# Kernel optimization log

Measured on AMD Instinct MI355X. Metric: run time of the kernel, lower is better.

The kernel has to match this reference:

```python
import jax, jax.numpy as jnp
import numpy as np

LEVELS = [(128, 128), (64, 64), (32, 32), (16, 16)]  # (H_l, W_l) per feature level
N_TOTAL = sum(h * w for h, w in LEVELS)  # 21760
B, D, H, P, L = 2, 256, 8, 4, 4
HD = D // H
FFN_DIM = 1024


def setup_inputs() -> dict:
    key = jax.random.key(0)
    ks = jax.random.split(key, 12)
    s = 0.02  # weight init scale
    return {
        'embed': jax.random.normal(ks[0], (B, N_TOTAL, D), jnp.float32),
        'pos': jax.random.normal(ks[1], (B, N_TOTAL, D), jnp.float32),
        'ref_points': jax.random.uniform(ks[2], (B, N_TOTAL, L, 2), jnp.float32),
        'ln1_w': jnp.ones((D,), jnp.float32), 'ln1_b': jnp.zeros((D,), jnp.float32),
        'ln2_w': jnp.ones((D,), jnp.float32), 'ln2_b': jnp.zeros((D,), jnp.float32),
        'Wv': jax.random.normal(ks[3], (D, D), jnp.float32) * s, 'bv': jnp.zeros((D,), jnp.float32),
        'Woff': jax.random.normal(ks[4], (D, H * L * P * 2), jnp.float32) * s, 'boff': jnp.zeros((H * L * P * 2,), jnp.float32),
        'Wattn': jax.random.normal(ks[5], (D, H * L * P), jnp.float32) * s, 'battn': jnp.zeros((H * L * P,), jnp.float32),
        'Wo': jax.random.normal(ks[6], (D, D), jnp.float32) * s, 'bo': jnp.zeros((D,), jnp.float32),
        'W1': jax.random.normal(ks[7], (D, FFN_DIM), jnp.float32) * s, 'b1': jnp.zeros((FFN_DIM,), jnp.float32),
        'W2': jax.random.normal(ks[8], (FFN_DIM, D), jnp.float32) * s, 'b2': jnp.zeros((D,), jnp.float32),
        'dimensions': jnp.array(LEVELS, jnp.int32),
    }


def _layer_norm(x, w, b):
    m = jnp.mean(x, axis=-1, keepdims=True)
    v = jnp.mean(jnp.square(x - m), axis=-1, keepdims=True)
    return (x - m) * jax.lax.rsqrt(v + 1e-5) * w + b


def _msda(q, ref, v, dims, Wv, bv, Woff, boff, Wattn, battn, Wo, bo):
    # q, v: (B, N, D); ref: (B, N, L, 2) normalized (x, y)
    Bq, N, _ = q.shape
    value = (v @ Wv + bv).reshape(Bq, N, H, HD)
    off = (q @ Woff + boff).reshape(Bq, N, H, L, P, 2)
    aw = jax.nn.softmax((q @ Wattn + battn).reshape(Bq, N, H, L * P), axis=-1)
    aw = aw.reshape(Bq, N, H, L, P)
    # offset normalizer is [W_l, H_l]
    norm = jnp.stack([dims[:, 1], dims[:, 0]], axis=-1).astype(q.dtype)  # (L, 2)
    loc = ref[:, :, None, :, None, :] + off / norm[None, None, None, :, None, :]  # (B,N,H,L,P,2)

    out = jnp.zeros((Bq, N, H, HD), q.dtype)
    start = 0
    for l, (Hl, Wl) in enumerate(LEVELS):
        S = Hl * Wl
        vl = value[:, start:start + S].transpose(0, 2, 1, 3)  # (B, H, S, hd)
        start += S
        # grid_sample semantics: align_corners=False, zero padding
        x = loc[:, :, :, l, :, 0] * Wl - 0.5  # (B, N, H, P)
        y = loc[:, :, :, l, :, 1] * Hl - 0.5
        x0 = jnp.floor(x); y0 = jnp.floor(y)
        wx = x - x0; wy = y - y0
        x0i = x0.astype(jnp.int32); y0i = y0.astype(jnp.int32)
        samp = jnp.zeros(x.shape + (HD,), q.dtype)
        for dy, dx, w in ((0, 0, (1 - wx) * (1 - wy)), (0, 1, wx * (1 - wy)),
                          (1, 0, (1 - wx) * wy), (1, 1, wx * wy)):
            xi = x0i + dx; yi = y0i + dy
            valid = (xi >= 0) & (xi < Wl) & (yi >= 0) & (yi < Hl)
            idx = jnp.clip(yi, 0, Hl - 1) * Wl + jnp.clip(xi, 0, Wl - 1)  # (B, N, H, P)
            idx_t = idx.transpose(0, 2, 1, 3).reshape(Bq, H, N * P)
            g = jnp.take_along_axis(vl, idx_t[..., None], axis=2)  # (B, H, N*P, hd)
            g = g.reshape(Bq, H, N, P, HD).transpose(0, 2, 1, 3, 4)  # (B, N, H, P, hd)
            samp = samp + (w * valid)[..., None] * g
        out = out + jnp.sum(samp * aw[:, :, :, l, :, None], axis=3)
    return out.reshape(Bq, N, D) @ Wo + bo


def reference(embed, pos, ref_points, ln1_w, ln1_b, ln2_w, ln2_b, Wv, bv, Woff, boff,
              Wattn, battn, Wo, bo, W1, b1, W2, b2, dimensions):
    v = _layer_norm(embed, ln1_w, ln1_b)
    q = v + pos
    embed = embed + _msda(q, ref_points, v, dimensions, Wv, bv, Woff, boff, Wattn, battn, Wo, bo)
    f = _layer_norm(embed, ln2_w, ln2_b)
    embed = embed + jax.nn.relu(f @ W1 + b1) @ W2 + b2
    return embed
```

## Files before the change

### kernel.cpp

```cpp
#include <hip/hip_runtime.h>
#include <cstdint>
#include <cstddef>

#define N_TOTAL 21760
#define BATCH   2
#define M_TOT   (BATCH * N_TOTAL)
#define DMODEL  256
#define NHEAD   8
#define HDIM    32
#define FFN     1024

typedef __bf16 b16x8 __attribute__((ext_vector_type(8)));
typedef float  f32x4 __attribute__((ext_vector_type(4)));

typedef const __attribute__((address_space(1))) void g_void;
typedef __attribute__((address_space(3))) void lds_void;

__device__ __forceinline__ unsigned short f2b(float f) {
  union { float f; unsigned u; } v; v.f = f;
  unsigned r = v.u + 0x7FFF + ((v.u >> 16) & 1);
  return (unsigned short)(r >> 16);
}
__device__ __forceinline__ float b2f(unsigned short u) {
  union { unsigned u; float f; } v; v.u = (unsigned)u << 16;
  return v.f;
}

__device__ __forceinline__ int xcd_wgid(int bid, int nwg) {
  int q = nwg >> 3, r = nwg & 7;
  int xcd = bid & 7, k = bid >> 3;
  return (xcd < r ? xcd * (q + 1) : r * (q + 1) + (xcd - r) * q) + k;
}

__global__ void wconv_all(const float* __restrict__ Wv, const float* __restrict__ Woff,
                          const float* __restrict__ Wattn, const float* __restrict__ Wo,
                          const float* __restrict__ W1, const float* __restrict__ W2,
                          unsigned short* __restrict__ dstbase) {
  int idx = blockIdx.x * 256 + threadIdx.x;
  const float* src; int K, N, off;
  if (idx < 65536)       { src = Wv;    K = 256;  N = 256;  off = 0;      }
  else if (idx < 131072) { src = Woff;  K = 256;  N = 256;  off = 65536;  idx -= 65536; }
  else if (idx < 163840) { src = Wattn; K = 256;  N = 128;  off = 131072; idx -= 131072; }
  else if (idx < 229376) { src = Wo;    K = 256;  N = 256;  off = 163840; idx -= 163840; }
  else if (idx < 491520) { src = W1;    K = 256;  N = 1024; off = 229376; idx -= 229376; }
  else if (idx < 753664) { src = W2;    K = 1024; N = 256;  off = 491520; idx -= 491520; }
  else return;
  int k = idx / N, n = idx - k * N;
  dstbase[off + (size_t)n * K + k] = f2b(src[idx]);
}

__global__ void ln1_kernel(const float* __restrict__ x, const float* __restrict__ pos,
                           const float* __restrict__ w, const float* __restrict__ b,
                           unsigned short* __restrict__ vb, unsigned short* __restrict__ qb) {
  int t = threadIdx.x;
  int tkn = blockIdx.x * 4 + (t >> 6);
  int lane = t & 63;
  size_t base = (size_t)tkn * DMODEL + lane * 4;
  float4 xv = *(const float4*)&x[base];
  float s1 = xv.x + xv.y + xv.z + xv.w;
  float s2 = xv.x * xv.x + xv.y * xv.y + xv.z * xv.z + xv.w * xv.w;
  #pragma unroll
  for (int off = 32; off; off >>= 1) {
    s1 += __shfl_down(s1, off);
    s2 += __shfl_down(s2, off);
  }
  s1 = __shfl(s1, 0); s2 = __shfl(s2, 0);
  float m   = s1 * (1.0f / DMODEL);
  float var = s2 * (1.0f / DMODEL) - m * m;
  float rs  = rsqrtf(var + 1e-5f);
  float4 wv = *(const float4*)&w[lane * 4];
  float4 bv = *(const float4*)&b[lane * 4];
  float4 pv = *(const float4*)&pos[base];
  float o0 = (xv.x - m) * rs * wv.x + bv.x;
  float o1 = (xv.y - m) * rs * wv.y + bv.y;
  float o2 = (xv.z - m) * rs * wv.z + bv.z;
  float o3 = (xv.w - m) * rs * wv.w + bv.w;
  ushort4 vo = {f2b(o0), f2b(o1), f2b(o2), f2b(o3)};
  ushort4 qo = {f2b(o0 + pv.x), f2b(o1 + pv.y), f2b(o2 + pv.z), f2b(o3 + pv.w)};
  *(ushort4*)&vb[base] = vo;
  *(ushort4*)&qb[base] = qo;
}

__device__ __forceinline__ void gemm_core(
    const unsigned short* __restrict__ A, const unsigned short* __restrict__ Bt,
    const float* __restrict__ bias,
    const float* __restrict__ addf, const unsigned short* __restrict__ addb,
    float* __restrict__ Cf, unsigned short* __restrict__ Cb,
    int K, int N, int relu, int row0, int col0,
    unsigned short* As, unsigned short* Bs) {
  int t  = threadIdx.x;
  int w  = t >> 6;
  int l  = t & 63;
  int wm = w >> 1, wn = w & 1;
  int lr = l & 15;
  int kq = l >> 4;

  f32x4 acc[4][4];
  #pragma unroll
  for (int i = 0; i < 4; ++i)
    #pragma unroll
    for (int j = 0; j < 4; ++j) acc[i][j] = (f32x4){0.f, 0.f, 0.f, 0.f};

  int srow = (l >> 3);
  int sseg = (l & 7) * 8;

  for (int k0 = 0; k0 < K; k0 += 64) {
    #pragma unroll
    for (int i = 0; i < 4; ++i) {
      int c = w * 4 + i;
      const unsigned short* ga = A  + (size_t)(row0 + c * 8 + srow) * K + k0 + sseg;
      const unsigned short* gb = Bt + (size_t)(col0 + c * 8 + srow) * K + k0 + sseg;
      __builtin_amdgcn_global_load_lds((g_void*)ga, (lds_void*)(As + c * 512), 16, 0, 0);
      __builtin_amdgcn_global_load_lds((g_void*)gb, (lds_void*)(Bs + c * 512), 16, 0, 0);
    }
    __syncthreads();
    #pragma unroll
    for (int kk = 0; kk < 2; ++kk) {
      b16x8 aF[4], bF[4];
      #pragma unroll
      for (int i = 0; i < 4; ++i)
        aF[i] = *(const b16x8*)&As[(wm * 64 + i * 16 + lr) * 64 + kk * 32 + kq * 8];
      #pragma unroll
      for (int j = 0; j < 4; ++j)
        bF[j] = *(const b16x8*)&Bs[(wn * 64 + j * 16 + lr) * 64 + kk * 32 + kq * 8];
      #pragma unroll
      for (int i = 0; i < 4; ++i)
        #pragma unroll
        for (int j = 0; j < 4; ++j)
          acc[i][j] = __builtin_amdgcn_mfma_f32_16x16x32_bf16(aF[i], bF[j], acc[i][j], 0, 0, 0);
    }
    __syncthreads();
  }

  #pragma unroll
  for (int j = 0; j < 4; ++j) {
    int colg = col0 + wn * 64 + j * 16 + lr;
    float bcol = bias[colg];
    #pragma unroll
    for (int i = 0; i < 4; ++i) {
      int r0g = row0 + wm * 64 + i * 16 + kq * 4;
      #pragma unroll
      for (int r = 0; r < 4; ++r) {
        int rowg = r0g + r;
        float o = acc[i][j][r] + bcol;
        if (relu) o = fmaxf(o, 0.0f);
        if (addf) o += addf[(size_t)rowg * N + colg];
        if (addb) o += b2f(addb[(size_t)rowg * N + colg]);
        if (Cf) Cf[(size_t)rowg * N + colg] = o;
        if (Cb) Cb[(size_t)rowg * N + colg] = f2b(o);
      }
    }
  }
}

__global__ __launch_bounds__(256, 3)
void gemm_bf16(const unsigned short* __restrict__ A,
               const unsigned short* __restrict__ Bt,
               const float* __restrict__ bias,
               const float* __restrict__ addf, const unsigned short* __restrict__ addb,
               float* __restrict__ Cf, unsigned short* __restrict__ Cb,
               int K, int N, int relu, int ncolt) {
  __shared__ unsigned short As[128 * 64];
  __shared__ unsigned short Bs[128 * 64];
  int wgid = xcd_wgid(blockIdx.x, gridDim.x);
  int row0 = (wgid / ncolt) * 128;
  int col0 = (wgid % ncolt) * 128;
  gemm_core(A, Bt, bias, addf, addb, Cf, Cb, K, N, relu, row0, col0, As, Bs);
}

__global__ __launch_bounds__(256, 3)
void gemm_proj(const unsigned short* __restrict__ vb,
               const unsigned short* __restrict__ qb,
               const unsigned short* __restrict__ Wvt,
               const unsigned short* __restrict__ Wofft,
               const unsigned short* __restrict__ Wattnt,
               const float* __restrict__ bv, const float* __restrict__ boff,
               const float* __restrict__ battn,
               unsigned short* __restrict__ valb,
               unsigned short* __restrict__ offb,
               unsigned short* __restrict__ awb) {
  __shared__ unsigned short As[128 * 64];
  __shared__ unsigned short Bs[128 * 64];
  int wgid = xcd_wgid(blockIdx.x, gridDim.x);
  int y = wgid % 5;
  int row0 = (wgid / 5) * 128;
  const unsigned short* A; const unsigned short* Bt; const float* bias;
  unsigned short* C; int col0, N;
  if (y < 2)      { A = vb; Bt = Wvt;    bias = bv;    C = valb; col0 = y * 128;       N = 256; }
  else if (y < 4) { A = qb; Bt = Wofft;  bias = boff;  C = offb; col0 = (y - 2) * 128; N = 256; }
  else            { A = qb; Bt = Wattnt; bias = battn; C = awb;  col0 = 0;             N = 128; }
  gemm_core(A, Bt, bias, nullptr, nullptr, nullptr, C, 256, N, 0, row0, col0, As, Bs);
}

__global__ __launch_bounds__(512, 2)
void gemm_wo_ln2(const unsigned short* __restrict__ A,
                 const unsigned short* __restrict__ Bt,
                 const float* __restrict__ bias,
                 const float* __restrict__ emb,
                 const float* __restrict__ lnw, const float* __restrict__ lnb,
                 unsigned short* __restrict__ emb2b,
                 unsigned short* __restrict__ fb16) {
  __shared__ unsigned short As[128 * 64];
  __shared__ unsigned short Bs[256 * 64];
  __shared__ float lnS1[128 * 4], lnS2[128 * 4];
  __shared__ float lnM[128], lnR[128];
  int t  = threadIdx.x;
  int w  = t >> 6;
  int l  = t & 63;
  int wm = w >> 2, wn = w & 3;
  int lr = l & 15;
  int kq = l >> 4;
  int row0 = xcd_wgid(blockIdx.x, gridDim.x) * 128;

  f32x4 acc[4][4];
  #pragma unroll
  for (int i = 0; i < 4; ++i)
    #pragma unroll
    for (int j = 0; j < 4; ++j) acc[i][j] = (f32x4){0.f, 0.f, 0.f, 0.f};

  int srow = (l >> 3);
  int sseg = (l & 7) * 8;

  for (int k0 = 0; k0 < 256; k0 += 64) {
    #pragma unroll
    for (int i = 0; i < 2; ++i) {
      int c = w * 2 + i;
      const unsigned short* ga = A + (size_t)(row0 + c * 8 + srow) * 256 + k0 + sseg;
      __builtin_amdgcn_global_load_lds((g_void*)ga, (lds_void*)(As + c * 512), 16, 0, 0);
    }
    #pragma unroll
    for (int i = 0; i < 4; ++i) {
      int c = w * 4 + i;
      const unsigned short* gb = Bt + (size_t)(c * 8 + srow) * 256 + k0 + sseg;
      __builtin_amdgcn_global_load_lds((g_void*)gb, (lds_void*)(Bs + c * 512), 16, 0, 0);
    }
    __syncthreads();
    #pragma unroll
    for (int kk = 0; kk < 2; ++kk) {
      b16x8 aF[4], bF[4];
      #pragma unroll
      for (int i = 0; i < 4; ++i)
        aF[i] = *(const b16x8*)&As[(wm * 64 + i * 16 + lr) * 64 + kk * 32 + kq * 8];
      #pragma unroll
      for (int j = 0; j < 4; ++j)
        bF[j] = *(const b16x8*)&Bs[(wn * 64 + j * 16 + lr) * 64 + kk * 32 + kq * 8];
      #pragma unroll
      for (int i = 0; i < 4; ++i)
        #pragma unroll
        for (int j = 0; j < 4; ++j)
          acc[i][j] = __builtin_amdgcn_mfma_f32_16x16x32_bf16(aF[i], bF[j], acc[i][j], 0, 0, 0);
    }
    __syncthreads();
  }

  float s1[4][4] = {}, s2[4][4] = {};
  #pragma unroll
  for (int j = 0; j < 4; ++j) {
    int colg = wn * 64 + j * 16 + lr;
    float bcol = bias[colg];
    #pragma unroll
    for (int i = 0; i < 4; ++i) {
      int rowg = row0 + wm * 64 + i * 16 + kq * 4;
      #pragma unroll
      for (int r = 0; r < 4; ++r) {
        float o = acc[i][j][r] + bcol + emb[(size_t)(rowg + r) * 256 + colg];
        acc[i][j][r] = o;
        s1[i][r] += o;
        s2[i][r] += o * o;
      }
    }
  }
  #pragma unroll
  for (int m = 1; m < 16; m <<= 1) {
    #pragma unroll
    for (int i = 0; i < 4; ++i)
      #pragma unroll
      for (int r = 0; r < 4; ++r) {
        s1[i][r] += __shfl_xor(s1[i][r], m);
        s2[i][r] += __shfl_xor(s2[i][r], m);
      }
  }
  if (lr == 0) {
    #pragma unroll
    for (int i = 0; i < 4; ++i)
      #pragma unroll
      for (int r = 0; r < 4; ++r) {
        int rl = wm * 64 + i * 16 + kq * 4 + r;
        lnS1[rl * 4 + wn] = s1[i][r];
        lnS2[rl * 4 + wn] = s2[i][r];
      }
  }
  __syncthreads();
  if (t < 128) {
    float a = lnS1[t * 4] + lnS1[t * 4 + 1] + lnS1[t * 4 + 2] + lnS1[t * 4 + 3];
    float b = lnS2[t * 4] + lnS2[t * 4 + 1] + lnS2[t * 4 + 2] + lnS2[t * 4 + 3];
    float m = a * (1.0f / 256.0f);
    float var = b * (1.0f / 256.0f) - m * m;
    lnM[t] = m;
    lnR[t] = rsqrtf(var + 1e-5f);
  }
  __syncthreads();
  #pragma unroll
  for (int i = 0; i < 4; ++i) {
    #pragma unroll
    for (int r = 0; r < 4; ++r) {
      int rl = wm * 64 + i * 16 + kq * 4 + r;
      float m = lnM[rl], rs = lnR[rl];
      int rowg = row0 + rl;
      #pragma unroll
      for (int j = 0; j < 4; ++j) {
        int colg = wn * 64 + j * 16 + lr;
        float o = acc[i][j][r];
        emb2b[(size_t)rowg * 256 + colg] = f2b(o);
        fb16[(size_t)rowg * 256 + colg] = f2b((o - m) * rs * lnw[colg] + lnb[colg]);
      }
    }
  }
}

__global__ void msda_kernel(const unsigned short* __restrict__ value,
                            const unsigned short* __restrict__ offb,
                            const unsigned short* __restrict__ awb,
                            const float* __restrict__ ref,
                            unsigned short* __restrict__ outb) {
  __shared__ int2 P[544] __attribute__((aligned(16)));
  int bid = blockIdx.x;
  int tkn = (bid & 7) * (M_TOT / 8) + (bid >> 3);
  int t   = threadIdx.x;
  int b   = (tkn >= N_TOTAL) ? 1 : 0;

  if (t < 128) {
    int h = t >> 4, s = t & 15, lev = s >> 2, p = s & 3;
    float lg = b2f(awb[(size_t)tkn * 128 + h * 16 + s]);
    float mx = lg;
    #pragma unroll
    for (int m = 1; m < 16; m <<= 1) mx = fmaxf(mx, __shfl_xor(mx, m, 16));
    float e = __expf(lg - mx);
    float sum = e;
    #pragma unroll
    for (int m = 1; m < 16; m <<= 1) sum += __shfl_xor(sum, m, 16);
    float aw = e / sum;

    const int HL[4] = {128, 64, 32, 16};
    const int ST[4] = {0, 16384, 20480, 21504};
    int Wl = HL[lev];
    float rx = ref[(size_t)tkn * 8 + lev * 2 + 0];
    float ry = ref[(size_t)tkn * 8 + lev * 2 + 1];
    float ox = b2f(offb[(size_t)tkn * 256 + h * 32 + lev * 8 + p * 2 + 0]);
    float oy = b2f(offb[(size_t)tkn * 256 + h * 32 + lev * 8 + p * 2 + 1]);
    float x = rx * (float)Wl + ox - 0.5f;
    float y = ry * (float)Wl + oy - 0.5f;
    float x0f = floorf(x), y0f = floorf(y);
    float wx = x - x0f, wy = y - y0f;
    int x0 = (int)x0f, y0 = (int)y0f;
    float wt[4] = {(1.f - wx) * (1.f - wy), wx * (1.f - wy),
                   (1.f - wx) * wy, wx * wy};
    int base = b * N_TOTAL + ST[lev];
    #pragma unroll
    for (int tp = 0; tp < 4; ++tp) {
      int e4 = s * 4 + tp;
      int idx = h * 68 + (e4 >> 5) * 34 + (e4 & 31);
      int xi = x0 + (tp & 1), yi = y0 + (tp >> 1);
      bool ok = (xi >= 0) & (xi < Wl) & (yi >= 0) & (yi < Wl);
      float wgt = ok ? aw * wt[tp] : 0.f;
      int boff2 = ok ? (((base + yi * Wl + xi) * 256 + h * 32) * 2) : 0;
      P[idx] = (int2){__float_as_int(wgt), boff2};
    }
  }
  __syncthreads();

  int h = t >> 5, g = t & 31, dp = g & 15, half = g >> 4;
  int o = h * 68 + half * 34;
  unsigned doff = dp * 4;
  const char* vbase = (const char*)value;
  float accL = 0.f, accH = 0.f;
  #pragma unroll 4
  for (int j2 = 0; j2 < 16; ++j2) {
    int4 pr2 = *(const int4*)&P[o + j2 * 2];
    float wgt0 = __int_as_float(pr2.x);
    float wgt1 = __int_as_float(pr2.z);
    unsigned v0 = *(const unsigned*)(vbase + (size_t)((unsigned)pr2.y + doff));
    unsigned v1 = *(const unsigned*)(vbase + (size_t)((unsigned)pr2.w + doff));
    union { unsigned u; float f; } l0, h0, l1, h1;
    l0.u = v0 << 16; h0.u = v0 & 0xffff0000u;
    l1.u = v1 << 16; h1.u = v1 & 0xffff0000u;
    accL += wgt0 * l0.f + wgt1 * l1.f;
    accH += wgt0 * h0.f + wgt1 * h1.f;
  }
  accL += __shfl_xor(accL, 16);
  accH += __shfl_xor(accH, 16);
  if (half == 0) {
    unsigned pk = (unsigned)f2b(accL) | ((unsigned)f2b(accH) << 16);
    *(unsigned*)&outb[(size_t)tkn * 256 + h * 32 + dp * 2] = pk;
  }
}

extern "C" void kernel_launch(void* const* d_in, const int* in_sizes, int n_in,
                              void* d_out, int out_size, void* d_ws, size_t ws_size,
                              hipStream_t stream) {
  const float* embed = (const float*)d_in[0];
  const float* pos   = (const float*)d_in[1];
  const float* refp  = (const float*)d_in[2];
  const float* ln1w  = (const float*)d_in[3];
  const float* ln1b  = (const float*)d_in[4];
  const float* ln2w  = (const float*)d_in[5];
  const float* ln2b  = (const float*)d_in[6];
  const float* Wv    = (const float*)d_in[7];
  const float* bv    = (const float*)d_in[8];
  const float* Woff  = (const float*)d_in[9];
  const float* boff  = (const float*)d_in[10];
  const float* Wattn = (const float*)d_in[11];
  const float* battn = (const float*)d_in[12];
  const float* Wo    = (const float*)d_in[13];
  const float* bo    = (const float*)d_in[14];
  const float* W1    = (const float*)d_in[15];
  const float* b1    = (const float*)d_in[16];
  const float* W2    = (const float*)d_in[17];
  const float* b2    = (const float*)d_in[18];
  float* out = (float*)d_out;
  float* ws  = (float*)d_ws;

  const size_t U = (size_t)M_TOT * DMODEL;
  unsigned short* valb16 = (unsigned short*)ws;
  unsigned short* offb16 = (unsigned short*)(ws + U / 2);
  unsigned short* awb16  = (unsigned short*)(ws + U);
  unsigned short* msdab  = (unsigned short*)(ws + U + U / 4);
  unsigned short* hid16  = (unsigned short*)ws;
  unsigned short* emb2b  = (unsigned short*)(ws + 2 * U);
  unsigned short* vb16   = (unsigned short*)(ws + 3 * U);
  unsigned short* qb16   = (unsigned short*)(ws + 3 * U + U / 2);
  unsigned short* fb16   = (unsigned short*)(ws + 4 * U);
  unsigned short* wbuf   = (unsigned short*)(ws + 4 * U + U / 2);

  unsigned short* Wvt    = wbuf;
  unsigned short* Wofft  = wbuf + 65536;
  unsigned short* Wattnt = wbuf + 131072;
  unsigned short* Wot    = wbuf + 163840;
  unsigned short* W1t    = wbuf + 229376;
  unsigned short* W2t    = wbuf + 491520;

  wconv_all<<<(753664 + 255) / 256, 256, 0, stream>>>(Wv, Woff, Wattn, Wo, W1, W2, wbuf);

  ln1_kernel<<<M_TOT / 4, 256, 0, stream>>>(embed, pos, ln1w, ln1b, vb16, qb16);

  gemm_proj<<<(M_TOT / 128) * 5, 256, 0, stream>>>(
      vb16, qb16, Wvt, Wofft, Wattnt, bv, boff, battn, valb16, offb16, awb16);

  msda_kernel<<<M_TOT, 256, 0, stream>>>(valb16, offb16, awb16, refp, msdab);

  gemm_wo_ln2<<<M_TOT / 128, 512, 0, stream>>>(
      msdab, Wot, bo, embed, ln2w, ln2b, emb2b, fb16);

  gemm_bf16<<<(M_TOT / 128) * 8, 256, 0, stream>>>(
      fb16, W1t, b1, nullptr, nullptr, nullptr, hid16, 256, 1024, 1, 8);
  gemm_bf16<<<(M_TOT / 128) * 2, 256, 0, stream>>>(
      hid16, W2t, b2, nullptr, emb2b, out, nullptr, 1024, 256, 0, 2);
}
```

Measured before the change: 301.3 us.

## Swizzle GEMM LDS tiles and stage bf16 epilogue through LDS for vector stores

Applies an XOR swizzle to the 16-byte segments of the A/B tiles in LDS, both on the global-to-LDS copy and on the MFMA fragment reads, to reduce LDS bank conflicts. The bf16-output epilogues of the generic, projection and Wo+LN2 GEMMs now write results into a swizzled LDS staging buffer and then emit coalesced 16-byte global stores instead of scattered 2-byte stores. This costs extra barriers and LDS traffic in the epilogue, and the Wo kernel's output pass runs in two halves per output tensor.

```diff
diff --git a/kernel.cpp b/kernel.cpp
--- a/kernel.cpp
+++ b/kernel.cpp
@@ -87,7 +87,9 @@
     const float* __restrict__ addf, const unsigned short* __restrict__ addb,
     float* __restrict__ Cf, unsigned short* __restrict__ Cb,
     int K, int N, int relu, int row0, int col0,
-    unsigned short* As, unsigned short* Bs) {
+    unsigned short* S ) {
+  unsigned short* As = S;
+  unsigned short* Bs = S + 8192;
   int t  = threadIdx.x;
   int w  = t >> 6;
   int l  = t & 63;
@@ -101,15 +103,15 @@
     #pragma unroll
     for (int j = 0; j < 4; ++j) acc[i][j] = (f32x4){0.f, 0.f, 0.f, 0.f};
 
-  int srow = (l >> 3);
-  int sseg = (l & 7) * 8;
+  int srow = l >> 3;
+  int swseg = ((l & 7) ^ srow) * 8;
 
   for (int k0 = 0; k0 < K; k0 += 64) {
     #pragma unroll
     for (int i = 0; i < 4; ++i) {
       int c = w * 4 + i;
-      const unsigned short* ga = A  + (size_t)(row0 + c * 8 + srow) * K + k0 + sseg;
-      const unsigned short* gb = Bt + (size_t)(col0 + c * 8 + srow) * K + k0 + sseg;
+      const unsigned short* ga = A  + (size_t)(row0 + c * 8 + srow) * K + k0 + swseg;
+      const unsigned short* gb = Bt + (size_t)(col0 + c * 8 + srow) * K + k0 + swseg;
       __builtin_amdgcn_global_load_lds((g_void*)ga, (lds_void*)(As + c * 512), 16, 0, 0);
       __builtin_amdgcn_global_load_lds((g_void*)gb, (lds_void*)(Bs + c * 512), 16, 0, 0);
     }
@@ -118,11 +120,17 @@
     for (int kk = 0; kk < 2; ++kk) {
       b16x8 aF[4], bF[4];
       #pragma unroll
-      for (int i = 0; i < 4; ++i)
-        aF[i] = *(const b16x8*)&As[(wm * 64 + i * 16 + lr) * 64 + kk * 32 + kq * 8];
-      #pragma unroll
-      for (int j = 0; j < 4; ++j)
-        bF[j] = *(const b16x8*)&Bs[(wn * 64 + j * 16 + lr) * 64 + kk * 32 + kq * 8];
+      for (int i = 0; i < 4; ++i) {
+        int row = wm * 64 + i * 16 + lr;
+        int gp = (kk * 4 + kq) ^ (lr & 7);
+        aF[i] = *(const b16x8*)&As[row * 64 + gp * 8];
+      }
+      #pragma unroll
+      for (int j = 0; j < 4; ++j) {
+        int row = wn * 64 + j * 16 + lr;
+        int gp = (kk * 4 + kq) ^ (lr & 7);
+        bF[j] = *(const b16x8*)&Bs[row * 64 + gp * 8];
+      }
       #pragma unroll
       for (int i = 0; i < 4; ++i)
         #pragma unroll
@@ -132,22 +140,51 @@
     __syncthreads();
   }
 
-  #pragma unroll
-  for (int j = 0; j < 4; ++j) {
-    int colg = col0 + wn * 64 + j * 16 + lr;
-    float bcol = bias[colg];
-    #pragma unroll
-    for (int i = 0; i < 4; ++i) {
-      int r0g = row0 + wm * 64 + i * 16 + kq * 4;
-      #pragma unroll
-      for (int r = 0; r < 4; ++r) {
-        int rowg = r0g + r;
-        float o = acc[i][j][r] + bcol;
-        if (relu) o = fmaxf(o, 0.0f);
-        if (addf) o += addf[(size_t)rowg * N + colg];
-        if (addb) o += b2f(addb[(size_t)rowg * N + colg]);
-        if (Cf) Cf[(size_t)rowg * N + colg] = o;
-        if (Cb) Cb[(size_t)rowg * N + colg] = f2b(o);
+  if (Cb) {
+    #pragma unroll
+    for (int j = 0; j < 4; ++j) {
+      int coll = wn * 64 + j * 16 + lr;
+      int colg = col0 + coll;
+      float bcol = bias[colg];
+      #pragma unroll
+      for (int i = 0; i < 4; ++i) {
+        int rl0 = wm * 64 + i * 16 + kq * 4;
+        #pragma unroll
+        for (int r = 0; r < 4; ++r) {
+          int rowl = rl0 + r;
+          float o = acc[i][j][r] + bcol;
+          if (relu) o = fmaxf(o, 0.0f);
+          if (addf) o += addf[(size_t)(row0 + rowl) * N + colg];
+          if (addb) o += b2f(addb[(size_t)(row0 + rowl) * N + colg]);
+          S[rowl * 128 + (coll ^ ((rowl & 3) << 5))] = f2b(o);
+        }
+      }
+    }
+    __syncthreads();
+    #pragma unroll
+    for (int m = 0; m < 8; ++m) {
+      int cc = m * 256 + t;
+      int row = cc >> 4, g = cc & 15;
+      float4 v = *(const float4*)&S[row * 128 + ((g ^ ((row & 3) << 2)) << 3)];
+      *(float4*)&Cb[(size_t)(row0 + row) * N + col0 + g * 8] = v;
+    }
+  } else {
+    #pragma unroll
+    for (int j = 0; j < 4; ++j) {
+      int colg = col0 + wn * 64 + j * 16 + lr;
+      float bcol = bias[colg];
+      #pragma unroll
+      for (int i = 0; i < 4; ++i) {
+        int r0g = row0 + wm * 64 + i * 16 + kq * 4;
+        #pragma unroll
+        for (int r = 0; r < 4; ++r) {
+          int rowg = r0g + r;
+          float o = acc[i][j][r] + bcol;
+          if (relu) o = fmaxf(o, 0.0f);
+          if (addf) o += addf[(size_t)rowg * N + colg];
+          if (addb) o += b2f(addb[(size_t)rowg * N + colg]);
+          Cf[(size_t)rowg * N + colg] = o;
+        }
       }
     }
   }
@@ -160,12 +197,11 @@
                const float* __restrict__ addf, const unsigned short* __restrict__ addb,
                float* __restrict__ Cf, unsigned short* __restrict__ Cb,
                int K, int N, int relu, int ncolt) {
-  __shared__ unsigned short As[128 * 64];
-  __shared__ unsigned short Bs[128 * 64];
+  __shared__ unsigned short S[16384];
   int wgid = xcd_wgid(blockIdx.x, gridDim.x);
   int row0 = (wgid / ncolt) * 128;
   int col0 = (wgid % ncolt) * 128;
-  gemm_core(A, Bt, bias, addf, addb, Cf, Cb, K, N, relu, row0, col0, As, Bs);
+  gemm_core(A, Bt, bias, addf, addb, Cf, Cb, K, N, relu, row0, col0, S);
 }
 
 __global__ __launch_bounds__(256, 3)
@@ -179,8 +215,7 @@
                unsigned short* __restrict__ valb,
                unsigned short* __restrict__ offb,
                unsigned short* __restrict__ awb) {
-  __shared__ unsigned short As[128 * 64];
-  __shared__ unsigned short Bs[128 * 64];
+  __shared__ unsigned short S[16384];
   int wgid = xcd_wgid(blockIdx.x, gridDim.x);
   int y = wgid % 5;
   int row0 = (wgid / 5) * 128;
@@ -189,7 +224,7 @@
   if (y < 2)      { A = vb; Bt = Wvt;    bias = bv;    C = valb; col0 = y * 128;       N = 256; }
   else if (y < 4) { A = qb; Bt = Wofft;  bias = boff;  C = offb; col0 = (y - 2) * 128; N = 256; }
   else            { A = qb; Bt = Wattnt; bias = battn; C = awb;  col0 = 0;             N = 128; }
-  gemm_core(A, Bt, bias, nullptr, nullptr, nullptr, C, 256, N, 0, row0, col0, As, Bs);
+  gemm_core(A, Bt, bias, nullptr, nullptr, nullptr, C, 256, N, 0, row0, col0, S);
 }
 
 __global__ __launch_bounds__(512, 2)
@@ -200,10 +235,11 @@
                  const float* __restrict__ lnw, const float* __restrict__ lnb,
                  unsigned short* __restrict__ emb2b,
                  unsigned short* __restrict__ fb16) {
-  __shared__ unsigned short As[128 * 64];
-  __shared__ unsigned short Bs[256 * 64];
+  __shared__ unsigned short S[24576];
   __shared__ float lnS1[128 * 4], lnS2[128 * 4];
   __shared__ float lnM[128], lnR[128];
+  unsigned short* As = S;
+  unsigned short* Bs = S + 8192;
   int t  = threadIdx.x;
   int w  = t >> 6;
   int l  = t & 63;
@@ -218,20 +254,20 @@
     #pragma unroll
     for (int j = 0; j < 4; ++j) acc[i][j] = (f32x4){0.f, 0.f, 0.f, 0.f};
 
-  int srow = (l >> 3);
-  int sseg = (l & 7) * 8;
+  int srow = l >> 3;
+  int swseg = ((l & 7) ^ srow) * 8;
 
   for (int k0 = 0; k0 < 256; k0 += 64) {
     #pragma unroll
     for (int i = 0; i < 2; ++i) {
       int c = w * 2 + i;
-      const unsigned short* ga = A + (size_t)(row0 + c * 8 + srow) * 256 + k0 + sseg;
+      const unsigned short* ga = A + (size_t)(row0 + c * 8 + srow) * 256 + k0 + swseg;
       __builtin_amdgcn_global_load_lds((g_void*)ga, (lds_void*)(As + c * 512), 16, 0, 0);
     }
     #pragma unroll
     for (int i = 0; i < 4; ++i) {
       int c = w * 4 + i;
-      const unsigned short* gb = Bt + (size_t)(c * 8 + srow) * 256 + k0 + sseg;
+      const unsigned short* gb = Bt + (size_t)(c * 8 + srow) * 256 + k0 + swseg;
       __builtin_amdgcn_global_load_lds((g_void*)gb, (lds_void*)(Bs + c * 512), 16, 0, 0);
     }
     __syncthreads();
@@ -239,11 +275,17 @@
     for (int kk = 0; kk < 2; ++kk) {
       b16x8 aF[4], bF[4];
       #pragma unroll
-      for (int i = 0; i < 4; ++i)
-        aF[i] = *(const b16x8*)&As[(wm * 64 + i * 16 + lr) * 64 + kk * 32 + kq * 8];
-      #pragma unroll
-      for (int j = 0; j < 4; ++j)
-        bF[j] = *(const b16x8*)&Bs[(wn * 64 + j * 16 + lr) * 64 + kk * 32 + kq * 8];
+      for (int i = 0; i < 4; ++i) {
+        int row = wm * 64 + i * 16 + lr;
+        int gp = (kk * 4 + kq) ^ (lr & 7);
+        aF[i] = *(const b16x8*)&As[row * 64 + gp * 8];
+      }
+      #pragma unroll
+      for (int j = 0; j < 4; ++j) {
+        int row = wn * 64 + j * 16 + lr;
+        int gp = (kk * 4 + kq) ^ (lr & 7);
+        bF[j] = *(const b16x8*)&Bs[row * 64 + gp * 8];
+      }
       #pragma unroll
       for (int i = 0; i < 4; ++i)
         #pragma unroll
@@ -300,19 +342,38 @@
     lnR[t] = rsqrtf(var + 1e-5f);
   }
   __syncthreads();
+
   #pragma unroll
-  for (int i = 0; i < 4; ++i) {
-    #pragma unroll
-    for (int r = 0; r < 4; ++r) {
-      int rl = wm * 64 + i * 16 + kq * 4 + r;
-      float m = lnM[rl], rs = lnR[rl];
-      int rowg = row0 + rl;
-      #pragma unroll
-      for (int j = 0; j < 4; ++j) {
-        int colg = wn * 64 + j * 16 + lr;
-        float o = acc[i][j][r];
-        emb2b[(size_t)rowg * 256 + colg] = f2b(o);
-        fb16[(size_t)rowg * 256 + colg] = f2b((o - m) * rs * lnw[colg] + lnb[colg]);
+  for (int outn = 0; outn < 2; ++outn) {
+    unsigned short* dst = outn == 0 ? emb2b : fb16;
+    #pragma unroll
+    for (int half = 0; half < 2; ++half) {
+      __syncthreads();
+      if ((wn >> 1) == half) {
+        #pragma unroll
+        for (int j = 0; j < 4; ++j) {
+          int colg = wn * 64 + j * 16 + lr;
+          int coll = colg - half * 128;
+          #pragma unroll
+          for (int i = 0; i < 4; ++i) {
+            #pragma unroll
+            for (int r = 0; r < 4; ++r) {
+              int rowl = wm * 64 + i * 16 + kq * 4 + r;
+              float o = acc[i][j][r];
+              float vv = outn == 0 ? o
+                  : (o - lnM[rowl]) * lnR[rowl] * lnw[colg] + lnb[colg];
+              S[rowl * 128 + (coll ^ ((rowl & 3) << 5))] = f2b(vv);
+            }
+          }
+        }
+      }
+      __syncthreads();
+      #pragma unroll
+      for (int m = 0; m < 4; ++m) {
+        int cc = m * 512 + t;
+        int row = cc >> 4, g = cc & 15;
+        float4 v = *(const float4*)&S[row * 128 + ((g ^ ((row & 3) << 2)) << 3)];
+        *(float4*)&dst[(size_t)(row0 + row) * 256 + half * 128 + g * 8] = v;
       }
     }
   }
```

After: 293.7 us. 2.5% less time.
